# Kernel optimization log

Measured on AMD Instinct MI355X. Metric: run time of the kernel, lower is better.

The kernel has to match this reference:

```python
import jax, jax.numpy as jnp
import numpy as np

N_NODES = 50000
N_EDGES = 800000
D_IN = 128
D_HID = 128
N_CLASSES = 10
N_GRAPHS = 64


def setup_inputs() -> dict:
    key = jax.random.key(0)
    ks = jax.random.split(key, 12)
    x = jax.random.normal(ks[0], (N_NODES, D_IN), dtype=jnp.float32)
    edge_index = jax.random.randint(ks[1], (2, N_EDGES), 0, N_NODES, dtype=jnp.int32)
    batch = jnp.sort(jax.random.randint(ks[2], (N_NODES,), 0, N_GRAPHS, dtype=jnp.int32))
    s = 0.05
    conv0_w = jax.random.normal(ks[3], (D_IN, D_HID), dtype=jnp.float32) * s
    conv0_b = jax.random.normal(ks[4], (D_HID,), dtype=jnp.float32) * s
    conv1_w = jax.random.normal(ks[5], (D_HID, D_HID), dtype=jnp.float32) * s
    conv1_b = jax.random.normal(ks[6], (D_HID,), dtype=jnp.float32) * s
    lin0_w = jax.random.normal(ks[7], (D_HID, D_HID), dtype=jnp.float32) * s
    lin0_b = jax.random.normal(ks[8], (D_HID,), dtype=jnp.float32) * s
    lin1_w = jax.random.normal(ks[9], (D_HID, N_CLASSES), dtype=jnp.float32) * s
    lin1_b = jax.random.normal(ks[10], (N_CLASSES,), dtype=jnp.float32) * s
    return dict(x=x, edge_index=edge_index, batch=batch,
                conv0_w=conv0_w, conv0_b=conv0_b,
                conv1_w=conv1_w, conv1_b=conv1_b,
                lin0_w=lin0_w, lin0_b=lin0_b,
                lin1_w=lin1_w, lin1_b=lin1_b)


def gcn_conv(x, edge_index, w, b):
    # PyG GCNConv: linear transform, add self-loops, D^-1/2 (A+I) D^-1/2 aggregation, + bias
    n = x.shape[0]
    h = x @ w  # [N, out]
    loop = jnp.arange(n, dtype=edge_index.dtype)
    row = jnp.concatenate([edge_index[0], loop])  # source nodes
    col = jnp.concatenate([edge_index[1], loop])  # destination nodes
    deg = jax.ops.segment_sum(jnp.ones_like(col, dtype=h.dtype), col, num_segments=n)
    dinv = jnp.where(deg > 0, jax.lax.rsqrt(deg), 0.0)
    norm = dinv[row] * dinv[col]  # [E+N]
    msg = h[row] * norm[:, None]  # gather + scale
    out = jax.ops.segment_sum(msg, col, num_segments=n)  # scatter-add
    return out + b


def reference(x, edge_index, batch, conv0_w, conv0_b, conv1_w, conv1_b,
              lin0_w, lin0_b, lin1_w, lin1_b):
    h = jax.nn.relu(gcn_conv(x, edge_index, conv0_w, conv0_b))
    h = jax.nn.relu(gcn_conv(h, edge_index, conv1_w, conv1_b))
    # global max pooling over nodes of each graph
    h = jax.ops.segment_max(h, batch, num_segments=N_GRAPHS)  # [G, D_HID]
    # NOTE: original applies relu after EVERY linear, including the output layer
    h = jax.nn.relu(h @ lin0_w + lin0_b)
    h = jax.nn.relu(h @ lin1_w + lin1_b)
    return jax.nn.log_softmax(h, axis=-1)
```

## Files before the change

### kernel.cpp

```cpp
#include <hip/hip_runtime.h>

#define D 128
#define BINCAP 6144
#define P2CAP 6144

typedef __attribute__((ext_vector_type(8))) short short8;
typedef __attribute__((ext_vector_type(4))) float f32x4;
typedef __attribute__((ext_vector_type(2))) float f32x2;

__device__ inline unsigned short f2bf(float f) {
    unsigned u = __float_as_uint(f);
    return (unsigned short)((u + 0x7FFFu + ((u >> 16) & 1u)) >> 16);
}
__device__ inline float bflo(unsigned u) { return __uint_as_float(u << 16); }
__device__ inline float bfhi(unsigned u) { return __uint_as_float(u & 0xFFFF0000u); }

__global__ __launch_bounds__(256) void k_initW(const float* __restrict__ w0, const float* __restrict__ w1,
                                               const float* __restrict__ b0, const float* __restrict__ b1,
                                               uint4* __restrict__ Wp0, uint4* __restrict__ Wp1,
                                               float* __restrict__ b0p, float* __restrict__ b1p,
                                               int* __restrict__ binCur, int* __restrict__ pool,
                                               unsigned* __restrict__ h0b, unsigned* __restrict__ h1b,
                                               int nbins, int n) {
    int t = threadIdx.x, b = blockIdx.x;
    int e = b * 256 + t;
    {
        int l = e & 63, U = (e >> 6) & 7, T = e >> 9;
        int nn = U * 16 + (l & 15);
        int kq = T * 32 + ((l >> 4) << 3);
        unsigned r[4], s[4];
#pragma unroll
        for (int jj = 0; jj < 4; ++jj) {
            int k0 = kq + 2 * jj, k1 = k0 + 1;
            unsigned a0 = f2bf(w0[k0 * 128 + nn]), a1 = f2bf(w0[k1 * 128 + nn]);
            r[jj] = a0 | (a1 << 16);
            int c0 = ((k0 & 7) << 4) | (k0 >> 3), c1 = ((k1 & 7) << 4) | (k1 >> 3);
            unsigned q0 = f2bf(w1[c0 * 128 + nn]), q1 = f2bf(w1[c1 * 128 + nn]);
            s[jj] = q0 | (q1 << 16);
        }
        Wp0[e] = make_uint4(r[0], r[1], r[2], r[3]);
        Wp1[e] = make_uint4(s[0], s[1], s[2], s[3]);
    }
    if (b == 0) {
        if (t < nbins) binCur[t] = t * BINCAP;
        for (int i = t; i < 64 * 128; i += 256) pool[i] = 0;
    }
    if (b == 1 && t < 128) {
        int c = ((t & 7) << 4) | (t >> 3);
        b0p[t] = b0[c];
        b1p[t] = b1[c];
    }
    if (b == 2 && t < 64) {
        h0b[(size_t)n * 64 + t] = 0u;
        h1b[(size_t)n * 64 + t] = 0u;
    }
}

__global__ __launch_bounds__(256) void k_p1scatter(const int* __restrict__ row, const int* __restrict__ col,
                                                   int* __restrict__ binCur, unsigned* __restrict__ ebuf, int E) {
    __shared__ int h[256], s[256], delta[256], lcur[256];
    __shared__ unsigned stage[4096];
    int t = threadIdx.x;
    h[t] = 0;
    __syncthreads();
    int base = blockIdx.x * 4096;
    int cnt = min(4096, E - base);
    if (cnt == 4096) {
        int myc[16], myr[16];
        const int4* c4 = (const int4*)(col + base);
        const int4* r4 = (const int4*)(row + base);
#pragma unroll
        for (int k = 0; k < 4; ++k) {
            int4 cv = c4[t * 4 + k];
            int4 rv = r4[t * 4 + k];
            myc[k * 4 + 0] = cv.x; myc[k * 4 + 1] = cv.y; myc[k * 4 + 2] = cv.z; myc[k * 4 + 3] = cv.w;
            myr[k * 4 + 0] = rv.x; myr[k * 4 + 1] = rv.y; myr[k * 4 + 2] = rv.z; myr[k * 4 + 3] = rv.w;
        }
#pragma unroll
        for (int k = 0; k < 16; ++k) atomicAdd(&h[myc[k] >> 8], 1);
        __syncthreads();
        int v = h[t];
        s[t] = v;
        __syncthreads();
        for (int off = 1; off < 256; off <<= 1) {
            int tmp = (t >= off) ? s[t - off] : 0;
            __syncthreads();
            s[t] += tmp;
            __syncthreads();
        }
        int excl = s[t] - v;
        lcur[t] = excl;
        delta[t] = (v > 0) ? (atomicAdd(&binCur[t], v) - excl) : 0;
        __syncthreads();
#pragma unroll
        for (int k = 0; k < 16; ++k) {
            int d = myc[k];
            int slot = atomicAdd(&lcur[d >> 8], 1);
            stage[slot] = ((unsigned)d << 16) | (unsigned)myr[k];
        }
        __syncthreads();
#pragma unroll
        for (int k = 0; k < 16; ++k) {
            int slot = k * 256 + t;
            unsigned vv = stage[slot];
            int b = vv >> 24;
            ebuf[delta[b] + slot] = vv;
        }
    } else {
        for (int k = 0; k < 16; ++k) {
            int e = base + k * 256 + t;
            if (e < E) atomicAdd(&h[col[e] >> 8], 1);
        }
        __syncthreads();
        int v = h[t];
        s[t] = v;
        __syncthreads();
        for (int off = 1; off < 256; off <<= 1) {
            int tmp = (t >= off) ? s[t - off] : 0;
            __syncthreads();
            s[t] += tmp;
            __syncthreads();
        }
        int excl = s[t] - v;
        lcur[t] = excl;
        delta[t] = (v > 0) ? (atomicAdd(&binCur[t], v) - excl) : 0;
        __syncthreads();
        for (int k = 0; k < 16; ++k) {
            int e = base + k * 256 + t;
            if (e < E) {
                int d = col[e];
                int slot = atomicAdd(&lcur[d >> 8], 1);
                stage[slot] = ((unsigned)d << 16) | (unsigned)row[e];
            }
        }
        __syncthreads();
        for (int k = 0; k < 16; ++k) {
            int slot = k * 256 + t;
            if (slot < cnt) {
                unsigned vv = stage[slot];
                int b = vv >> 24;
                ebuf[delta[b] + slot] = vv;
            }
        }
    }
}

__global__ __launch_bounds__(256) void k_p2sort(const unsigned* __restrict__ ebuf, const int* __restrict__ binCur,
                                                int* __restrict__ csr, int* __restrict__ off_, int* __restrict__ end_,
                                                float* __restrict__ dinv, int n) {
    __shared__ unsigned stage[P2CAP];
    __shared__ unsigned stage2[P2CAP];
    __shared__ int h[256], s[256], cur[256];
    int b = blockIdx.x, t = threadIdx.x;
    int beg = b * BINCAP;
    int cnt = binCur[b] - beg;
    h[t] = 0;
    __syncthreads();
    int nfull = cnt >> 2;
    const uint4* e4 = (const uint4*)(ebuf + beg);
    uint4* st4 = (uint4*)stage;
    for (int i = t; i < nfull; i += 256) {
        uint4 v = e4[i];
        st4[i] = v;
        atomicAdd(&h[(v.x >> 16) & 0xFF], 1);
        atomicAdd(&h[(v.y >> 16) & 0xFF], 1);
        atomicAdd(&h[(v.z >> 16) & 0xFF], 1);
        atomicAdd(&h[(v.w >> 16) & 0xFF], 1);
    }
    for (int i = (nfull << 2) + t; i < cnt; i += 256) {
        unsigned v = ebuf[beg + i];
        stage[i] = v;
        atomicAdd(&h[(v >> 16) & 0xFF], 1);
    }
    __syncthreads();
    int v = h[t];
    s[t] = v;
    __syncthreads();
    for (int off = 1; off < 256; off <<= 1) {
        int tmp = (t >= off) ? s[t - off] : 0;
        __syncthreads();
        s[t] += tmp;
        __syncthreads();
    }
    int excl = s[t] - v;
    cur[t] = excl;
    int d = b * 256 + t;
    if (d < n) {
        off_[d] = beg + excl;
        end_[d] = beg + excl + v;
        dinv[d] = rsqrtf((float)(v + 1));
    }
    __syncthreads();
    for (int i = t; i < cnt; i += 256) {
        unsigned vv = stage[i];
        int slot = atomicAdd(&cur[(vv >> 16) & 0xFF], 1);
        stage2[slot] = vv & 0xFFFFu;
    }
    __syncthreads();
    uint4* c4o = (uint4*)(csr + beg);
    uint4* st24 = (uint4*)stage2;
    for (int i = t; i < nfull; i += 256) c4o[i] = st24[i];
    for (int i = (nfull << 2) + t; i < cnt; i += 256) csr[beg + i] = (int)stage2[i];
}

__global__ __launch_bounds__(256) void k_gemm0(const float* __restrict__ x, const uint4* __restrict__ Wp,
                                               const float* __restrict__ dinv, unsigned* __restrict__ outb, int n) {
    int wave = threadIdx.x >> 6, l = threadIdx.x & 63;
    int mt = blockIdx.x * 4 + wave;
    int r0 = mt * 16;
    if (r0 >= n) return;
    int rowA = r0 + (l & 15);
    int kq = (l >> 4) * 8;
    f32x4 acc[8];
#pragma unroll
    for (int U = 0; U < 8; ++U) acc[U] = (f32x4){0.f, 0.f, 0.f, 0.f};
    const float* xr = x + (size_t)rowA * 128 + kq;
#pragma unroll
    for (int T = 0; T < 4; ++T) {
        float4 a0 = *(const float4*)(xr + T * 32);
        float4 a1 = *(const float4*)(xr + T * 32 + 4);
        short8 af;
        af[0] = (short)f2bf(a0.x); af[1] = (short)f2bf(a0.y);
        af[2] = (short)f2bf(a0.z); af[3] = (short)f2bf(a0.w);
        af[4] = (short)f2bf(a1.x); af[5] = (short)f2bf(a1.y);
        af[6] = (short)f2bf(a1.z); af[7] = (short)f2bf(a1.w);
#pragma unroll
        for (int U = 0; U < 8; ++U) {
            short8 bf = *(const short8*)&Wp[(T * 8 + U) * 64 + l];
            acc[U] = __builtin_amdgcn_mfma_f32_16x16x32_bf16(af, bf, acc[U], 0, 0, 0);
        }
    }
    int rq = l >> 4, cl = l & 15;
#pragma unroll
    for (int q = 0; q < 4; ++q) {
        int rr = r0 + rq * 4 + q;
        float d = dinv[rr];
        uint4 w;
        w.x = (unsigned)f2bf(acc[0][q] * d) | ((unsigned)f2bf(acc[1][q] * d) << 16);
        w.y = (unsigned)f2bf(acc[2][q] * d) | ((unsigned)f2bf(acc[3][q] * d) << 16);
        w.z = (unsigned)f2bf(acc[4][q] * d) | ((unsigned)f2bf(acc[5][q] * d) << 16);
        w.w = (unsigned)f2bf(acc[6][q] * d) | ((unsigned)f2bf(acc[7][q] * d) << 16);
        *(uint4*)(outb + (size_t)rr * 64 + cl * 4) = w;
    }
}

__device__ inline void gather8(const uint4* __restrict__ hp4, const int* __restrict__ csr,
                               int q, int beg, int len, int ZR, f32x2 acc[4]) {
    int maxlen = len;
    maxlen = max(maxlen, __shfl_xor(maxlen, 16, 64));
    maxlen = max(maxlen, __shfl_xor(maxlen, 32, 64));
    if (maxlen <= 0) return;
    int lm1 = len - 1;
    int s[8];
#pragma unroll
    for (int k = 0; k < 8; ++k) {
        int cv = csr[beg + min(k, lm1)];
        s[k] = (k < len) ? cv : ZR;
    }
    for (int j = 0; j < maxlen; j += 8) {
        uint4 u0 = hp4[(size_t)s[0] * 16 + q];
        uint4 u1 = hp4[(size_t)s[1] * 16 + q];
        uint4 u2 = hp4[(size_t)s[2] * 16 + q];
        uint4 u3 = hp4[(size_t)s[3] * 16 + q];
        uint4 u4 = hp4[(size_t)s[4] * 16 + q];
        uint4 u5 = hp4[(size_t)s[5] * 16 + q];
        uint4 u6 = hp4[(size_t)s[6] * 16 + q];
        uint4 u7 = hp4[(size_t)s[7] * 16 + q];
        int jn = j + 8;
        if (jn < maxlen) {
#pragma unroll
            for (int k = 0; k < 8; ++k) {
                int cv = csr[beg + min(jn + k, lm1)];
                s[k] = (jn + k < len) ? cv : ZR;
            }
        }
#define ACC8(U)                                                     \
        { f32x2 t0, t1, t2, t3;                                     \
          t0[0] = bflo(U.x); t0[1] = bfhi(U.x);                     \
          t1[0] = bflo(U.y); t1[1] = bfhi(U.y);                     \
          t2[0] = bflo(U.z); t2[1] = bfhi(U.z);                     \
          t3[0] = bflo(U.w); t3[1] = bfhi(U.w);                     \
          acc[0] += t0; acc[1] += t1; acc[2] += t2; acc[3] += t3; }
        ACC8(u0) ACC8(u1) ACC8(u2) ACC8(u3)
        ACC8(u4) ACC8(u5) ACC8(u6) ACC8(u7)
#undef ACC8
    }
}

__global__ __launch_bounds__(256) void k_aggemm(const unsigned* __restrict__ hp, const int* __restrict__ off_,
                                                const int* __restrict__ end_, const int* __restrict__ csr,
                                                const float* __restrict__ dinv, const float* __restrict__ bp,
                                                const uint4* __restrict__ Wp, unsigned* __restrict__ outb, int n) {
    __shared__ uint4 sA[16 * 17];
    int w = threadIdx.x >> 6, l = threadIdx.x & 63;
    int g = l >> 4, q = l & 15;
    int r0 = blockIdx.x * 16;
    int node = r0 + w * 4 + g;
    const uint4* hp4 = (const uint4*)hp;
    f32x2 acc[4];
    uint4 us = hp4[(size_t)node * 16 + q];
    acc[0][0] = bflo(us.x); acc[0][1] = bfhi(us.x);
    acc[1][0] = bflo(us.y); acc[1][1] = bfhi(us.y);
    acc[2][0] = bflo(us.z); acc[2][1] = bfhi(us.z);
    acc[3][0] = bflo(us.w); acc[3][1] = bfhi(us.w);
    int beg = off_[node];
    int len = end_[node] - beg;
    gather8(hp4, csr, q, beg, len, n, acc);
    float d0 = dinv[node];
    const float4* bp4 = (const float4*)bp;
    float4 ba = bp4[q * 2], bb = bp4[q * 2 + 1];
    uint4 pk;
    pk.x = (unsigned)f2bf(fmaxf(fmaf(d0, acc[0][0], ba.x), 0.f)) | ((unsigned)f2bf(fmaxf(fmaf(d0, acc[0][1], ba.y), 0.f)) << 16);
    pk.y = (unsigned)f2bf(fmaxf(fmaf(d0, acc[1][0], ba.z), 0.f)) | ((unsigned)f2bf(fmaxf(fmaf(d0, acc[1][1], ba.w), 0.f)) << 16);
    pk.z = (unsigned)f2bf(fmaxf(fmaf(d0, acc[2][0], bb.x), 0.f)) | ((unsigned)f2bf(fmaxf(fmaf(d0, acc[2][1], bb.y), 0.f)) << 16);
    pk.w = (unsigned)f2bf(fmaxf(fmaf(d0, acc[3][0], bb.z), 0.f)) | ((unsigned)f2bf(fmaxf(fmaf(d0, acc[3][1], bb.w), 0.f)) << 16);
    sA[(w * 4 + g) * 17 + q] = pk;
    __syncthreads();
    int rq = l >> 4, cl = l & 15;
    f32x4 c0v = (f32x4){0.f, 0.f, 0.f, 0.f}, c1v = (f32x4){0.f, 0.f, 0.f, 0.f};
#pragma unroll
    for (int T = 0; T < 4; ++T) {
        short8 af = *(const short8*)&sA[(l & 15) * 17 + T * 4 + rq];
        short8 bf0 = *(const short8*)&Wp[(T * 8 + 2 * w) * 64 + l];
        short8 bf1 = *(const short8*)&Wp[(T * 8 + 2 * w + 1) * 64 + l];
        c0v = __builtin_amdgcn_mfma_f32_16x16x32_bf16(af, bf0, c0v, 0, 0, 0);
        c1v = __builtin_amdgcn_mfma_f32_16x16x32_bf16(af, bf1, c1v, 0, 0, 0);
    }
#pragma unroll
    for (int qq = 0; qq < 4; ++qq) {
        int rr = r0 + rq * 4 + qq;
        float d2 = dinv[rr];
        unsigned pkk = (unsigned)f2bf(c0v[qq] * d2) | ((unsigned)f2bf(c1v[qq] * d2) << 16);
        outb[(size_t)rr * 64 + cl * 4 + w] = pkk;
    }
}

__global__ __launch_bounds__(256) void k_agg1(const unsigned* __restrict__ hp, const int* __restrict__ off_,
                                              const int* __restrict__ end_, const int* __restrict__ csr,
                                              const float* __restrict__ dinv, const float* __restrict__ bp,
                                              const int* __restrict__ batch, int* __restrict__ pool, int n) {
    __shared__ float2 sv[16][64];
    __shared__ int sg[16];
    int w = threadIdx.x >> 6, l = threadIdx.x & 63;
    int g = l >> 4, q = l & 15;
    int node = blockIdx.x * 16 + w * 4 + g;
    const uint4* hp4 = (const uint4*)hp;
    f32x2 acc[4];
    uint4 us = hp4[(size_t)node * 16 + q];
    acc[0][0] = bflo(us.x); acc[0][1] = bfhi(us.x);
    acc[1][0] = bflo(us.y); acc[1][1] = bfhi(us.y);
    acc[2][0] = bflo(us.z); acc[2][1] = bfhi(us.z);
    acc[3][0] = bflo(us.w); acc[3][1] = bfhi(us.w);
    int beg = off_[node];
    int len = end_[node] - beg;
    gather8(hp4, csr, q, beg, len, n, acc);
    float d0 = dinv[node];
    const float4* bp4 = (const float4*)bp;
    float4 ba = bp4[q * 2], bb = bp4[q * 2 + 1];
    int rowi = w * 4 + g;
    sv[rowi][q * 4 + 0] = make_float2(fmaxf(fmaf(d0, acc[0][0], ba.x), 0.f), fmaxf(fmaf(d0, acc[0][1], ba.y), 0.f));
    sv[rowi][q * 4 + 1] = make_float2(fmaxf(fmaf(d0, acc[1][0], ba.z), 0.f), fmaxf(fmaf(d0, acc[1][1], ba.w), 0.f));
    sv[rowi][q * 4 + 2] = make_float2(fmaxf(fmaf(d0, acc[2][0], bb.x), 0.f), fmaxf(fmaf(d0, acc[2][1], bb.y), 0.f));
    sv[rowi][q * 4 + 3] = make_float2(fmaxf(fmaf(d0, acc[3][0], bb.z), 0.f), fmaxf(fmaf(d0, acc[3][1], bb.w), 0.f));
    if (q == 0) sg[rowi] = batch[node];
    __syncthreads();
    if (threadIdx.x < 64) {
        int t = threadIdx.x;
        int c0 = 32 * (t & 3) + (t >> 2);
        int cur = sg[0];
        float2 m = sv[0][t];
        for (int ww = 1; ww < 16; ++ww) {
            int gg = sg[ww];
            float2 vv = sv[ww][t];
            if (gg == cur) { m.x = fmaxf(m.x, vv.x); m.y = fmaxf(m.y, vv.y); }
            else {
                atomicMax(&pool[cur * 128 + c0], __float_as_int(m.x));
                atomicMax(&pool[cur * 128 + c0 + 16], __float_as_int(m.y));
                cur = gg; m = vv;
            }
        }
        atomicMax(&pool[cur * 128 + c0], __float_as_int(m.x));
        atomicMax(&pool[cur * 128 + c0 + 16], __float_as_int(m.y));
    }
}

__global__ __launch_bounds__(128) void k_mlp(const float* __restrict__ pool, const float* __restrict__ W0,
                                             const float* __restrict__ b0, const float* __restrict__ W1,
                                             const float* __restrict__ b1, float* __restrict__ out) {
    __shared__ float rowv[128];
    __shared__ float h2[128];
    __shared__ float h3[10];
    int g = blockIdx.x, t = threadIdx.x;
    rowv[t] = pool[g * 128 + t];
    __syncthreads();
    float acc = b0[t];
    for (int k = 0; k < 128; ++k) acc = fmaf(rowv[k], W0[k * 128 + t], acc);
    h2[t] = fmaxf(acc, 0.f);
    __syncthreads();
    if (t < 10) {
        float a = b1[t];
        for (int k = 0; k < 128; ++k) a = fmaf(h2[k], W1[k * 10 + t], a);
        h3[t] = fmaxf(a, 0.f);
    }
    __syncthreads();
    if (t == 0) {
        float mx = h3[0];
        for (int j = 1; j < 10; ++j) mx = fmaxf(mx, h3[j]);
        float s = 0.f;
        for (int j = 0; j < 10; ++j) s += expf(h3[j] - mx);
        float lse = logf(s) + mx;
        for (int j = 0; j < 10; ++j) out[g * 10 + j] = h3[j] - lse;
    }
}

extern "C" void kernel_launch(void* const* d_in, const int* in_sizes, int n_in,
                              void* d_out, int out_size, void* d_ws, size_t ws_size,
                              hipStream_t stream) {
    const float* x   = (const float*)d_in[0];
    const int* eidx  = (const int*)d_in[1];
    const int* batch = (const int*)d_in[2];
    const float* w0  = (const float*)d_in[3];
    const float* b0  = (const float*)d_in[4];
    const float* w1  = (const float*)d_in[5];
    const float* b1  = (const float*)d_in[6];
    const float* lw0 = (const float*)d_in[7];
    const float* lb0 = (const float*)d_in[8];
    const float* lw1 = (const float*)d_in[9];
    const float* lb1 = (const float*)d_in[10];
    float* out = (float*)d_out;

    int n = in_sizes[2];
    int E = in_sizes[1] / 2;
    const int* row = eidx;
    const int* col = eidx + E;
    int nbins = (n + 255) >> 8;
    int nb1 = (E + 4095) / 4096;

    char* ws = (char*)d_ws;
    size_t o = 0;
    auto take = [&](size_t bytes) { void* p = ws + o; o += (bytes + 255) & ~(size_t)255; return p; };
    int*      binCur   = (int*)     take(256 * 4);
    int*      off_     = (int*)     take((size_t)n * 4);
    int*      end_     = (int*)     take((size_t)n * 4);
    float*    dinv     = (float*)   take((size_t)n * 4);
    int*      csrA     = (int*)     take(((size_t)nbins * BINCAP + 128) * 4);
    int*      csr      = csrA + 64;
    unsigned* ebuf     = (unsigned*)take(((size_t)nbins * BINCAP + 64) * 4);
    uint4*    Wp0      = (uint4*)   take(2048 * 16);
    uint4*    Wp1      = (uint4*)   take(2048 * 16);
    float*    b0p      = (float*)   take(128 * 4);
    float*    b1p      = (float*)   take(128 * 4);
    unsigned* h0b      = (unsigned*)take((size_t)(n + 1) * 64 * 4);
    unsigned* h1b      = (unsigned*)take((size_t)(n + 1) * 64 * 4);
    int*      pool     = (int*)     take(64 * 128 * 4);

    k_initW<<<8, 256, 0, stream>>>(w0, w1, b0, b1, Wp0, Wp1, b0p, b1p, binCur, pool, h0b, h1b, nbins, n);
    k_p1scatter<<<nb1, 256, 0, stream>>>(row, col, binCur, ebuf, E);
    k_p2sort<<<nbins, 256, 0, stream>>>(ebuf, binCur, csr, off_, end_, dinv, n);

    int mtBlocks = ((n + 15) / 16 + 3) / 4;

    k_gemm0<<<mtBlocks, 256, 0, stream>>>(x, Wp0, dinv, h0b, n);
    k_aggemm<<<n / 16, 256, 0, stream>>>(h0b, off_, end_, csr, dinv, b0p, Wp1, h1b, n);
    k_agg1<<<n / 16, 256, 0, stream>>>(h1b, off_, end_, csr, dinv, b1p, batch, pool, n);
    k_mlp<<<64, 128, 0, stream>>>((const float*)pool, lw0, lb0, lw1, lb1, out);
}
```

Measured before the change: 181.1 us.

## Replace two-pass binned sort with global atomic histogram, scan, scatter CSR build

Replaces the two-level binned radix-style CSR construction (block-local bucketing into fixed-capacity bins, then per-bin sort in LDS) with a three-kernel counting sort: a global atomic degree histogram, a per-block scan that recomputes its prefix by summing all earlier degrees, and an atomic-cursor scatter into the CSR. The aim is simpler kernels and a compact CSR without fixed-size bins. In exchange it uses many global atomics, does quadratic redundant work in the scan, and makes neighbour order within each row nondeterministic.

Result: slower. 281.1 us (+55.2%).

```diff
diff --git a/kernel.cpp b/kernel.cpp
--- a/kernel.cpp
+++ b/kernel.cpp
@@ -1,8 +1,6 @@
 #include <hip/hip_runtime.h>
 
 #define D 128
-#define BINCAP 6144
-#define P2CAP 6144
 
 typedef __attribute__((ext_vector_type(8))) short short8;
 typedef __attribute__((ext_vector_type(4))) float f32x4;
@@ -19,9 +17,9 @@
                                                const float* __restrict__ b0, const float* __restrict__ b1,
                                                uint4* __restrict__ Wp0, uint4* __restrict__ Wp1,
                                                float* __restrict__ b0p, float* __restrict__ b1p,
-                                               int* __restrict__ binCur, int* __restrict__ pool,
+                                               int* __restrict__ deg, int* __restrict__ pool,
                                                unsigned* __restrict__ h0b, unsigned* __restrict__ h1b,
-                                               int nbins, int n) {
+                                               int n) {
     int t = threadIdx.x, b = blockIdx.x;
     int e = b * 256 + t;
     {
@@ -41,8 +39,8 @@
         Wp0[e] = make_uint4(r[0], r[1], r[2], r[3]);
         Wp1[e] = make_uint4(s[0], s[1], s[2], s[3]);
     }
+    for (int i = e; i < n; i += 2048) deg[i] = 0;
     if (b == 0) {
-        if (t < nbins) binCur[t] = t * BINCAP;
         for (int i = t; i < 64 * 128; i += 256) pool[i] = 0;
     }
     if (b == 1 && t < 128) {
@@ -56,151 +54,76 @@
     }
 }
 
-__global__ __launch_bounds__(256) void k_p1scatter(const int* __restrict__ row, const int* __restrict__ col,
-                                                   int* __restrict__ binCur, unsigned* __restrict__ ebuf, int E) {
-    __shared__ int h[256], s[256], delta[256], lcur[256];
-    __shared__ unsigned stage[4096];
-    int t = threadIdx.x;
-    h[t] = 0;
-    __syncthreads();
-    int base = blockIdx.x * 4096;
-    int cnt = min(4096, E - base);
-    if (cnt == 4096) {
-        int myc[16], myr[16];
-        const int4* c4 = (const int4*)(col + base);
-        const int4* r4 = (const int4*)(row + base);
-#pragma unroll
-        for (int k = 0; k < 4; ++k) {
-            int4 cv = c4[t * 4 + k];
-            int4 rv = r4[t * 4 + k];
-            myc[k * 4 + 0] = cv.x; myc[k * 4 + 1] = cv.y; myc[k * 4 + 2] = cv.z; myc[k * 4 + 3] = cv.w;
-            myr[k * 4 + 0] = rv.x; myr[k * 4 + 1] = rv.y; myr[k * 4 + 2] = rv.z; myr[k * 4 + 3] = rv.w;
-        }
-#pragma unroll
-        for (int k = 0; k < 16; ++k) atomicAdd(&h[myc[k] >> 8], 1);
-        __syncthreads();
-        int v = h[t];
-        s[t] = v;
-        __syncthreads();
-        for (int off = 1; off < 256; off <<= 1) {
-            int tmp = (t >= off) ? s[t - off] : 0;
-            __syncthreads();
-            s[t] += tmp;
-            __syncthreads();
-        }
-        int excl = s[t] - v;
-        lcur[t] = excl;
-        delta[t] = (v > 0) ? (atomicAdd(&binCur[t], v) - excl) : 0;
-        __syncthreads();
-#pragma unroll
-        for (int k = 0; k < 16; ++k) {
-            int d = myc[k];
-            int slot = atomicAdd(&lcur[d >> 8], 1);
-            stage[slot] = ((unsigned)d << 16) | (unsigned)myr[k];
-        }
-        __syncthreads();
-#pragma unroll
-        for (int k = 0; k < 16; ++k) {
-            int slot = k * 256 + t;
-            unsigned vv = stage[slot];
-            int b = vv >> 24;
-            ebuf[delta[b] + slot] = vv;
-        }
-    } else {
-        for (int k = 0; k < 16; ++k) {
-            int e = base + k * 256 + t;
-            if (e < E) atomicAdd(&h[col[e] >> 8], 1);
-        }
-        __syncthreads();
-        int v = h[t];
-        s[t] = v;
-        __syncthreads();
-        for (int off = 1; off < 256; off <<= 1) {
-            int tmp = (t >= off) ? s[t - off] : 0;
-            __syncthreads();
-            s[t] += tmp;
-            __syncthreads();
-        }
-        int excl = s[t] - v;
-        lcur[t] = excl;
-        delta[t] = (v > 0) ? (atomicAdd(&binCur[t], v) - excl) : 0;
-        __syncthreads();
-        for (int k = 0; k < 16; ++k) {
-            int e = base + k * 256 + t;
-            if (e < E) {
-                int d = col[e];
-                int slot = atomicAdd(&lcur[d >> 8], 1);
-                stage[slot] = ((unsigned)d << 16) | (unsigned)row[e];
-            }
-        }
-        __syncthreads();
-        for (int k = 0; k < 16; ++k) {
-            int slot = k * 256 + t;
-            if (slot < cnt) {
-                unsigned vv = stage[slot];
-                int b = vv >> 24;
-                ebuf[delta[b] + slot] = vv;
-            }
-        }
-    }
-}
-
-__global__ __launch_bounds__(256) void k_p2sort(const unsigned* __restrict__ ebuf, const int* __restrict__ binCur,
-                                                int* __restrict__ csr, int* __restrict__ off_, int* __restrict__ end_,
-                                                float* __restrict__ dinv, int n) {
-    __shared__ unsigned stage[P2CAP];
-    __shared__ unsigned stage2[P2CAP];
-    __shared__ int h[256], s[256], cur[256];
+__global__ __launch_bounds__(256) void k_hist(const int* __restrict__ col, int* __restrict__ deg, int E) {
+    int i = blockIdx.x * 256 + threadIdx.x;
+    int nq = E >> 2;
+    if (i < nq) {
+        int4 c = ((const int4*)col)[i];
+        atomicAdd(&deg[c.x], 1);
+        atomicAdd(&deg[c.y], 1);
+        atomicAdd(&deg[c.z], 1);
+        atomicAdd(&deg[c.w], 1);
+    }
+    int rem = nq << 2;
+    int j = rem + i;
+    if (j < E && i < E - rem) atomicAdd(&deg[col[j]], 1);
+}
+
+__global__ __launch_bounds__(256) void k_scan(const int* __restrict__ deg, int* __restrict__ off_,
+                                              int* __restrict__ end_, int* __restrict__ cur,
+                                              float* __restrict__ dinv, int n) {
+    __shared__ int ws[4];
+    __shared__ int wt[4];
+    __shared__ int bb;
     int b = blockIdx.x, t = threadIdx.x;
-    int beg = b * BINCAP;
-    int cnt = binCur[b] - beg;
-    h[t] = 0;
-    __syncthreads();
-    int nfull = cnt >> 2;
-    const uint4* e4 = (const uint4*)(ebuf + beg);
-    uint4* st4 = (uint4*)stage;
-    for (int i = t; i < nfull; i += 256) {
-        uint4 v = e4[i];
-        st4[i] = v;
-        atomicAdd(&h[(v.x >> 16) & 0xFF], 1);
-        atomicAdd(&h[(v.y >> 16) & 0xFF], 1);
-        atomicAdd(&h[(v.z >> 16) & 0xFF], 1);
-        atomicAdd(&h[(v.w >> 16) & 0xFF], 1);
-    }
-    for (int i = (nfull << 2) + t; i < cnt; i += 256) {
-        unsigned v = ebuf[beg + i];
-        stage[i] = v;
-        atomicAdd(&h[(v >> 16) & 0xFF], 1);
-    }
-    __syncthreads();
-    int v = h[t];
-    s[t] = v;
-    __syncthreads();
-    for (int off = 1; off < 256; off <<= 1) {
-        int tmp = (t >= off) ? s[t - off] : 0;
-        __syncthreads();
-        s[t] += tmp;
-        __syncthreads();
-    }
-    int excl = s[t] - v;
-    cur[t] = excl;
-    int d = b * 256 + t;
+    int w = t >> 6, l = t & 63;
+    int base0 = b * 256;
+    int psum = 0;
+    for (int j = t; j < base0; j += 256) psum += deg[j];
+#pragma unroll
+    for (int o = 32; o > 0; o >>= 1) psum += __shfl_down(psum, o, 64);
+    if (l == 0) ws[w] = psum;
+    __syncthreads();
+    if (t == 0) bb = ws[0] + ws[1] + ws[2] + ws[3];
+    int d = base0 + t;
+    int v = (d < n) ? deg[d] : 0;
+    int inc = v;
+#pragma unroll
+    for (int o = 1; o < 64; o <<= 1) {
+        int x = __shfl_up(inc, o, 64);
+        if (l >= o) inc += x;
+    }
+    if (l == 63) wt[w] = inc;
+    __syncthreads();
+    int wbase = 0;
+    for (int j = 0; j < w; ++j) wbase += wt[j];
+    int excl = bb + wbase + (inc - v);
     if (d < n) {
-        off_[d] = beg + excl;
-        end_[d] = beg + excl + v;
+        off_[d] = excl;
+        end_[d] = excl + v;
+        cur[d]  = excl;
         dinv[d] = rsqrtf((float)(v + 1));
     }
-    __syncthreads();
-    for (int i = t; i < cnt; i += 256) {
-        unsigned vv = stage[i];
-        int slot = atomicAdd(&cur[(vv >> 16) & 0xFF], 1);
-        stage2[slot] = vv & 0xFFFFu;
-    }
-    __syncthreads();
-    uint4* c4o = (uint4*)(csr + beg);
-    uint4* st24 = (uint4*)stage2;
-    for (int i = t; i < nfull; i += 256) c4o[i] = st24[i];
-    for (int i = (nfull << 2) + t; i < cnt; i += 256) csr[beg + i] = (int)stage2[i];
+}
+
+__global__ __launch_bounds__(256) void k_scatter(const int* __restrict__ row, const int* __restrict__ col,
+                                                 int* __restrict__ cur, int* __restrict__ csr, int E) {
+    int i = blockIdx.x * 256 + threadIdx.x;
+    int nq = E >> 2;
+    if (i < nq) {
+        int4 c = ((const int4*)col)[i];
+        int4 r = ((const int4*)row)[i];
+        int p0 = atomicAdd(&cur[c.x], 1); csr[p0] = r.x;
+        int p1 = atomicAdd(&cur[c.y], 1); csr[p1] = r.y;
+        int p2 = atomicAdd(&cur[c.z], 1); csr[p2] = r.z;
+        int p3 = atomicAdd(&cur[c.w], 1); csr[p3] = r.w;
+    }
+    int rem = nq << 2;
+    int j = rem + i;
+    if (j < E && i < E - rem) {
+        int p = atomicAdd(&cur[col[j]], 1);
+        csr[p] = row[j];
+    }
 }
 
 __global__ __launch_bounds__(256) void k_gemm0(const float* __restrict__ x, const uint4* __restrict__ Wp,
@@ -433,19 +356,19 @@
     int E = in_sizes[1] / 2;
     const int* row = eidx;
     const int* col = eidx + E;
-    int nbins = (n + 255) >> 8;
-    int nb1 = (E + 4095) / 4096;
+    int nblkN = (n + 255) >> 8;
+    int nblkE = ((E >> 2) + 255) >> 8;
 
     char* ws = (char*)d_ws;
     size_t o = 0;
     auto take = [&](size_t bytes) { void* p = ws + o; o += (bytes + 255) & ~(size_t)255; return p; };
-    int*      binCur   = (int*)     take(256 * 4);
+    int*      deg      = (int*)     take((size_t)n * 4);
     int*      off_     = (int*)     take((size_t)n * 4);
     int*      end_     = (int*)     take((size_t)n * 4);
+    int*      cur      = (int*)     take((size_t)n * 4);
     float*    dinv     = (float*)   take((size_t)n * 4);
-    int*      csrA     = (int*)     take(((size_t)nbins * BINCAP + 128) * 4);
+    int*      csrA     = (int*)     take(((size_t)E + 128) * 4);
     int*      csr      = csrA + 64;
-    unsigned* ebuf     = (unsigned*)take(((size_t)nbins * BINCAP + 64) * 4);
     uint4*    Wp0      = (uint4*)   take(2048 * 16);
     uint4*    Wp1      = (uint4*)   take(2048 * 16);
     float*    b0p      = (float*)   take(128 * 4);
@@ -454,9 +377,10 @@
     unsigned* h1b      = (unsigned*)take((size_t)(n + 1) * 64 * 4);
     int*      pool     = (int*)     take(64 * 128 * 4);
 
-    k_initW<<<8, 256, 0, stream>>>(w0, w1, b0, b1, Wp0, Wp1, b0p, b1p, binCur, pool, h0b, h1b, nbins, n);
-    k_p1scatter<<<nb1, 256, 0, stream>>>(row, col, binCur, ebuf, E);
-    k_p2sort<<<nbins, 256, 0, stream>>>(ebuf, binCur, csr, off_, end_, dinv, n);
+    k_initW<<<8, 256, 0, stream>>>(w0, w1, b0, b1, Wp0, Wp1, b0p, b1p, deg, pool, h0b, h1b, n);
+    k_hist<<<nblkE, 256, 0, stream>>>(col, deg, E);
+    k_scan<<<nblkN, 256, 0, stream>>>(deg, off_, end_, cur, dinv, n);
+    k_scatter<<<nblkE, 256, 0, stream>>>(row, col, cur, csr, E);
 
     int mtBlocks = ((n + 15) / 16 + 3) / 4;
 
```

## Reorder nodes by degree to balance aggregation work across waves

Applied to the files above, without the earlier changes.

Builds a degree histogram in the sort kernel, then uses a scan kernel and a permutation kernel to make a node order bucketed by in-degree. The two aggregation kernels then process nodes in that order, so the four nodes sharing a wave have similar neighbour counts and the gather loops diverge less. In exchange it adds two kernel launches and one indirection per node. Nodes in a block are no longer contiguous, so output writes and the per-graph max-pool atomics lose locality, since consecutive nodes no longer share a graph.

Result: slower. 192.7 us (+6.4%).

```diff
diff --git a/kernel.cpp b/kernel.cpp
--- a/kernel.cpp
+++ b/kernel.cpp
@@ -21,7 +21,7 @@
                                                float* __restrict__ b0p, float* __restrict__ b1p,
                                                int* __restrict__ binCur, int* __restrict__ pool,
                                                unsigned* __restrict__ h0b, unsigned* __restrict__ h1b,
-                                               int nbins, int n) {
+                                               int* __restrict__ dhist, int nbins, int n) {
     int t = threadIdx.x, b = blockIdx.x;
     int e = b * 256 + t;
     {
@@ -54,6 +54,7 @@
         h0b[(size_t)n * 64 + t] = 0u;
         h1b[(size_t)n * 64 + t] = 0u;
     }
+    if (b == 3) dhist[t] = 0;
 }
 
 __global__ __launch_bounds__(256) void k_p1scatter(const int* __restrict__ row, const int* __restrict__ col,
@@ -147,14 +148,15 @@
 
 __global__ __launch_bounds__(256) void k_p2sort(const unsigned* __restrict__ ebuf, const int* __restrict__ binCur,
                                                 int* __restrict__ csr, int* __restrict__ off_, int* __restrict__ end_,
-                                                float* __restrict__ dinv, int n) {
+                                                float* __restrict__ dinv, int* __restrict__ dhist, int n) {
     __shared__ unsigned stage[P2CAP];
     __shared__ unsigned stage2[P2CAP];
-    __shared__ int h[256], s[256], cur[256];
+    __shared__ int h[256], s[256], cur[256], hd[256];
     int b = blockIdx.x, t = threadIdx.x;
     int beg = b * BINCAP;
     int cnt = binCur[b] - beg;
     h[t] = 0;
+    hd[t] = 0;
     __syncthreads();
     int nfull = cnt >> 2;
     const uint4* e4 = (const uint4*)(ebuf + beg);
@@ -189,8 +191,10 @@
         off_[d] = beg + excl;
         end_[d] = beg + excl + v;
         dinv[d] = rsqrtf((float)(v + 1));
-    }
-    __syncthreads();
+        atomicAdd(&hd[min(v, 255)], 1);
+    }
+    __syncthreads();
+    if (hd[t] > 0) atomicAdd(&dhist[t], hd[t]);
     for (int i = t; i < cnt; i += 256) {
         unsigned vv = stage[i];
         int slot = atomicAdd(&cur[(vv >> 16) & 0xFF], 1);
@@ -201,6 +205,44 @@
     uint4* st24 = (uint4*)stage2;
     for (int i = t; i < nfull; i += 256) c4o[i] = st24[i];
     for (int i = (nfull << 2) + t; i < cnt; i += 256) csr[beg + i] = (int)stage2[i];
+}
+
+__global__ __launch_bounds__(256) void k_dscan(const int* __restrict__ dhist, int* __restrict__ dcur) {
+    __shared__ int wt[4];
+    int t = threadIdx.x, w = t >> 6, l = t & 63;
+    int v = dhist[t], inc = v;
+#pragma unroll
+    for (int o = 1; o < 64; o <<= 1) {
+        int x = __shfl_up(inc, o, 64);
+        if (l >= o) inc += x;
+    }
+    if (l == 63) wt[w] = inc;
+    __syncthreads();
+    int wbase = 0;
+    for (int j = 0; j < w; ++j) wbase += wt[j];
+    dcur[t] = wbase + inc - v;
+}
+
+__global__ __launch_bounds__(256) void k_dperm(const int* __restrict__ off_, const int* __restrict__ end_,
+                                               int* __restrict__ dcur, int* __restrict__ perm, int n) {
+    __shared__ int h[256], base[256], lcur[256];
+    int b = blockIdx.x, t = threadIdx.x;
+    h[t] = 0; lcur[t] = 0;
+    __syncthreads();
+    int d = b * 256 + t;
+    int v = 0;
+    bool ok = (d < n);
+    if (ok) {
+        v = min(end_[d] - off_[d], 255);
+        atomicAdd(&h[v], 1);
+    }
+    __syncthreads();
+    if (h[t] > 0) base[t] = atomicAdd(&dcur[t], h[t]);
+    __syncthreads();
+    if (ok) {
+        int lo = atomicAdd(&lcur[v], 1);
+        perm[base[v] + lo] = d;
+    }
 }
 
 __global__ __launch_bounds__(256) void k_gemm0(const float* __restrict__ x, const uint4* __restrict__ Wp,
@@ -290,12 +332,13 @@
 __global__ __launch_bounds__(256) void k_aggemm(const unsigned* __restrict__ hp, const int* __restrict__ off_,
                                                 const int* __restrict__ end_, const int* __restrict__ csr,
                                                 const float* __restrict__ dinv, const float* __restrict__ bp,
-                                                const uint4* __restrict__ Wp, unsigned* __restrict__ outb, int n) {
+                                                const uint4* __restrict__ Wp, const int* __restrict__ perm,
+                                                unsigned* __restrict__ outb, int n) {
     __shared__ uint4 sA[16 * 17];
     int w = threadIdx.x >> 6, l = threadIdx.x & 63;
     int g = l >> 4, q = l & 15;
     int r0 = blockIdx.x * 16;
-    int node = r0 + w * 4 + g;
+    int node = perm[r0 + w * 4 + g];
     const uint4* hp4 = (const uint4*)hp;
     f32x2 acc[4];
     uint4 us = hp4[(size_t)node * 16 + q];
@@ -328,22 +371,23 @@
     }
 #pragma unroll
     for (int qq = 0; qq < 4; ++qq) {
-        int rr = r0 + rq * 4 + qq;
-        float d2 = dinv[rr];
+        int pn = perm[r0 + rq * 4 + qq];
+        float d2 = dinv[pn];
         unsigned pkk = (unsigned)f2bf(c0v[qq] * d2) | ((unsigned)f2bf(c1v[qq] * d2) << 16);
-        outb[(size_t)rr * 64 + cl * 4 + w] = pkk;
+        outb[(size_t)pn * 64 + cl * 4 + w] = pkk;
     }
 }
 
 __global__ __launch_bounds__(256) void k_agg1(const unsigned* __restrict__ hp, const int* __restrict__ off_,
                                               const int* __restrict__ end_, const int* __restrict__ csr,
                                               const float* __restrict__ dinv, const float* __restrict__ bp,
-                                              const int* __restrict__ batch, int* __restrict__ pool, int n) {
+                                              const int* __restrict__ batch, const int* __restrict__ perm,
+                                              int* __restrict__ pool, int n) {
     __shared__ float2 sv[16][64];
     __shared__ int sg[16];
     int w = threadIdx.x >> 6, l = threadIdx.x & 63;
     int g = l >> 4, q = l & 15;
-    int node = blockIdx.x * 16 + w * 4 + g;
+    int node = perm[blockIdx.x * 16 + w * 4 + g];
     const uint4* hp4 = (const uint4*)hp;
     f32x2 acc[4];
     uint4 us = hp4[(size_t)node * 16 + q];
@@ -443,6 +487,9 @@
     int*      off_     = (int*)     take((size_t)n * 4);
     int*      end_     = (int*)     take((size_t)n * 4);
     float*    dinv     = (float*)   take((size_t)n * 4);
+    int*      dhist    = (int*)     take(256 * 4);
+    int*      dcur     = (int*)     take(256 * 4);
+    int*      perm     = (int*)     take((size_t)n * 4);
     int*      csrA     = (int*)     take(((size_t)nbins * BINCAP + 128) * 4);
     int*      csr      = csrA + 64;
     unsigned* ebuf     = (unsigned*)take(((size_t)nbins * BINCAP + 64) * 4);
@@ -454,14 +501,16 @@
     unsigned* h1b      = (unsigned*)take((size_t)(n + 1) * 64 * 4);
     int*      pool     = (int*)     take(64 * 128 * 4);
 
-    k_initW<<<8, 256, 0, stream>>>(w0, w1, b0, b1, Wp0, Wp1, b0p, b1p, binCur, pool, h0b, h1b, nbins, n);
+    k_initW<<<8, 256, 0, stream>>>(w0, w1, b0, b1, Wp0, Wp1, b0p, b1p, binCur, pool, h0b, h1b, dhist, nbins, n);
     k_p1scatter<<<nb1, 256, 0, stream>>>(row, col, binCur, ebuf, E);
-    k_p2sort<<<nbins, 256, 0, stream>>>(ebuf, binCur, csr, off_, end_, dinv, n);
+    k_p2sort<<<nbins, 256, 0, stream>>>(ebuf, binCur, csr, off_, end_, dinv, dhist, n);
+    k_dscan<<<1, 256, 0, stream>>>(dhist, dcur);
+    k_dperm<<<nbins, 256, 0, stream>>>(off_, end_, dcur, perm, n);
 
     int mtBlocks = ((n + 15) / 16 + 3) / 4;
 
     k_gemm0<<<mtBlocks, 256, 0, stream>>>(x, Wp0, dinv, h0b, n);
-    k_aggemm<<<n / 16, 256, 0, stream>>>(h0b, off_, end_, csr, dinv, b0p, Wp1, h1b, n);
-    k_agg1<<<n / 16, 256, 0, stream>>>(h1b, off_, end_, csr, dinv, b1p, batch, pool, n);
+    k_aggemm<<<n / 16, 256, 0, stream>>>(h0b, off_, end_, csr, dinv, b0p, Wp1, perm, h1b, n);
+    k_agg1<<<n / 16, 256, 0, stream>>>(h1b, off_, end_, csr, dinv, b1p, batch, perm, pool, n);
     k_mlp<<<64, 128, 0, stream>>>((const float*)pool, lw0, lb0, lw1, lb1, out);
 }
```
